# Kernel tuning notes

Measured on AMD Instinct MI355X. Metric: run time of the kernel, lower is better.

## Reference

```python
import jax, jax.numpy as jnp
import numpy as np

N = 50000       # nodes
E = 400000      # edges (before self-loops)
IN_C = 128
HID = 32        # hidden_channels per head
HEADS = 8
OUT_C = 64
K = 16          # num_clusters
NEG_SLOPE = 0.2
EPS = 1e-16


def setup_inputs() -> dict:
    key = jax.random.key(0)
    ks = jax.random.split(key, 14)
    g = lambda k, sh, sc: (jax.random.normal(k, sh, jnp.float32) * sc)
    return {
        "x": jax.random.normal(ks[0], (N, IN_C), jnp.float32),
        "edge_index": jax.random.randint(ks[1], (2, E), 0, N, dtype=jnp.int32),
        # GAT layer 1: in -> HEADS*HID
        "W1": g(ks[2], (IN_C, HEADS * HID), 0.08),
        "att_src1": g(ks[3], (HEADS, HID), 0.1),
        "att_dst1": g(ks[4], (HEADS, HID), 0.1),
        "b1": jnp.zeros((HEADS * HID,), jnp.float32),
        # GAT layer 2: HEADS*HID -> OUT_C, heads=1, concat=False
        "W2": g(ks[5], (HEADS * HID, OUT_C), 0.06),
        "att_src2": g(ks[6], (1, OUT_C), 0.1),
        "att_dst2": g(ks[7], (1, OUT_C), 0.1),
        "b2": jnp.zeros((OUT_C,), jnp.float32),
        # MLP head: OUT_C -> 128 -> K
        "Wm1": g(ks[8], (OUT_C, 128), 0.1),
        "bm1": jnp.zeros((128,), jnp.float32),
        "Wm2": g(ks[9], (128, K), 0.1),
        "bm2": jnp.zeros((K,), jnp.float32),
    }


def _gat_layer(x, W, att_src, att_dst, bias, src, dst, heads, ch, concat):
    # x: [N, F_in] -> h: [N, H, C]
    h = (x @ W).reshape(N, heads, ch)
    a_src = jnp.einsum('nhc,hc->nh', h, att_src)   # [N, H]
    a_dst = jnp.einsum('nhc,hc->nh', h, att_dst)   # [N, H]
    e = jax.nn.leaky_relu(a_src[src] + a_dst[dst], NEG_SLOPE)  # [Etot, H]
    # segment softmax over destination node
    m = jax.ops.segment_max(e, dst, num_segments=N)            # [N, H]
    ex = jnp.exp(e - m[dst])
    den = jax.ops.segment_sum(ex, dst, num_segments=N)         # [N, H]
    alpha = ex / (den[dst] + EPS)                              # [Etot, H]
    out = jax.ops.segment_sum(alpha[:, :, None] * h[src], dst, num_segments=N)  # [N, H, C]
    out = out.reshape(N, heads * ch) if concat else out.mean(axis=1)
    return out + bias


def reference(x, edge_index, W1, att_src1, att_dst1, b1, W2, att_src2, att_dst2, b2, Wm1, bm1, Wm2, bm2):
    # PyG GATConv adds self-loops by default
    loop = jnp.arange(N, dtype=edge_index.dtype)
    src = jnp.concatenate([edge_index[0], loop])
    dst = jnp.concatenate([edge_index[1], loop])
    # dropout layers are identity in eval mode
    h = jax.nn.elu(_gat_layer(x, W1, att_src1, att_dst1, b1, src, dst, HEADS, HID, True))
    embeddings = _gat_layer(h, W2, att_src2, att_dst2, b2, src, dst, 1, OUT_C, False)
    logits = jax.nn.relu(embeddings @ Wm1 + bm1) @ Wm2 + bm2
    s = jax.nn.softmax(logits, axis=1)
    return (s, embeddings)
```

## Files before the change

kernel.cpp:

```cpp
#include <hip/hip_runtime.h>
#include <hip/hip_fp16.h>
#include <math.h>

#define NNODES 50000
#define NEDGES 400000
#define INC    128
#define HC1    256
#define NHEADS 8
#define OUTC   64
#define NK     16
#define NEG_SLOPE 0.2f
#define EPS_F  1e-16f

typedef unsigned short u16;
typedef __attribute__((ext_vector_type(8))) short bf16x8;
typedef __attribute__((ext_vector_type(4))) float f32x4;

__device__ __forceinline__ float lrelu(float x){ return x > 0.f ? x : NEG_SLOPE * x; }
__device__ __forceinline__ float eluf(float x){ return x > 0.f ? x : (__expf(x) - 1.f); }
__device__ __forceinline__ float bf2f(u16 v){ return __uint_as_float((unsigned)v << 16); }
__device__ __forceinline__ u16 f2bf(float f){
    unsigned u = __float_as_uint(f);
    unsigned r = (u + 0x7FFFu + ((u >> 16) & 1u)) >> 16;
    return (u16)r;
}
__device__ __forceinline__ short f2bf_s(float f){ return (short)f2bf(f); }
__device__ __forceinline__ u16 f2h(float f){ return __half_as_ushort(__float2half(f)); }
__device__ __forceinline__ float h2f(u16 v){ return __half2float(__ushort_as_half(v)); }

__device__ __forceinline__ void fmix_lo(float& acc, unsigned w, float a){
    asm("v_fma_mix_f32 %0, %1, %2, %0 op_sel:[0,0,0] op_sel_hi:[1,0,0]"
        : "+v"(acc) : "v"(w), "v"(a));
}
__device__ __forceinline__ void fmix_hi(float& acc, unsigned w, float a){
    asm("v_fma_mix_f32 %0, %1, %2, %0 op_sel:[1,0,0] op_sel_hi:[1,0,0]"
        : "+v"(acc) : "v"(w), "v"(a));
}
__device__ __forceinline__ void mac8(float* acc, uint4 w, float a){
    fmix_lo(acc[0], w.x, a); fmix_hi(acc[1], w.x, a);
    fmix_lo(acc[2], w.y, a); fmix_hi(acc[3], w.y, a);
    fmix_lo(acc[4], w.z, a); fmix_hi(acc[5], w.z, a);
    fmix_lo(acc[6], w.w, a); fmix_hi(acc[7], w.w, a);
}
__device__ __forceinline__ void mac4(float4& acc, uint2 w, float a){
    fmix_lo(acc.x, w.x, a); fmix_hi(acc.y, w.x, a);
    fmix_lo(acc.z, w.y, a); fmix_hi(acc.w, w.y, a);
}

#define EB 1563
#define TB 232
__global__ void count_deg_tw_k(const int* __restrict__ dst, int* __restrict__ deg,
                               const float* __restrict__ W1, u16* __restrict__ W1t,
                               const float* __restrict__ W2, u16* __restrict__ W2t,
                               const float* __restrict__ Wm1, u16* __restrict__ W1mt,
                               const float* __restrict__ Wm2, u16* __restrict__ W2mt){
    if (blockIdx.x < EB){
        int e = blockIdx.x * 256 + threadIdx.x;
        if (e < NEDGES) atomicAdd(&deg[dst[e]], 1);
    } else {
        int i = (blockIdx.x - EB) * 256 + threadIdx.x;
        if (i < 32768){
            int n = i >> 7, k = i & 127;
            W1t[i] = f2bf(W1[k * 256 + n]);
        } else if (i < 49152){
            int ii = i - 32768;
            int n = ii >> 8, k = ii & 255;
            W2t[ii] = f2bf(W2[k * 64 + n]);
        } else if (i < 57344){
            int ii = i - 49152;
            int hd = ii >> 6, e = ii & 63;
            W1mt[ii] = f2bf(Wm1[e * 128 + hd]);
        } else if (i < 59392){
            int ii = i - 57344;
            int k = ii >> 7, hd = ii & 127;
            W2mt[ii] = f2bf(Wm2[hd * NK + k]);
        }
    }
}

__global__ void blocksum_k(const int* __restrict__ deg, int* __restrict__ bsum){
    __shared__ int sm[4];
    int i = blockIdx.x * 256 + threadIdx.x;
    int v = (i < NNODES) ? deg[i] : 0;
    for (int off = 1; off < 64; off <<= 1) v += __shfl_xor(v, off);
    int lane = threadIdx.x & 63, wid = threadIdx.x >> 6;
    if (lane == 0) sm[wid] = v;
    __syncthreads();
    if (threadIdx.x == 0) bsum[blockIdx.x] = sm[0] + sm[1] + sm[2] + sm[3];
}

__global__ void scan_write_k(const int* __restrict__ deg, const int* __restrict__ bsum,
                             int* __restrict__ rowptr){
    __shared__ int sm[4];
    __shared__ int sadd;
    int tid = threadIdx.x;
    int pv = (tid < blockIdx.x) ? bsum[tid] : 0;
    for (int off = 1; off < 64; off <<= 1) pv += __shfl_xor(pv, off);
    int lane = tid & 63, wid = tid >> 6;
    if (lane == 0) sm[wid] = pv;
    __syncthreads();
    if (tid == 0) sadd = sm[0] + sm[1] + sm[2] + sm[3];
    __syncthreads();

    int i = blockIdx.x * 256 + tid;
    int v = (i < NNODES) ? deg[i] : 0;
    int sv = v;
    for (int off = 1; off < 64; off <<= 1){ int t = __shfl_up(sv, off); if (lane >= off) sv += t; }
    __shared__ int wsum[4];
    if (lane == 63) wsum[wid] = sv;
    __syncthreads();
    int add = sadd;
    for (int w = 0; w < wid; w++) add += wsum[w];
    sv += add;
    if (i < NNODES) rowptr[i + 1] = sv;
    if (i == 0) rowptr[0] = 0;
}

__global__ void fill_csr_k(const int* __restrict__ src, const int* __restrict__ dst,
                           const int* __restrict__ rowptr, int* __restrict__ fillc,
                           int* __restrict__ col){
    int e = blockIdx.x * 256 + threadIdx.x;
    if (e < NEDGES){
        int d = dst[e];
        int pos = atomicAdd(&fillc[d], 1);
        col[rowptr[d] + pos] = src[e];
    }
}

__global__ __launch_bounds__(256, 4) void l1_k(const float* __restrict__ x, const u16* __restrict__ W1t,
                     const float* __restrict__ att_s, const float* __restrict__ att_d,
                     u16* __restrict__ h1b, float* __restrict__ as1, float* __restrict__ ad1){
    __shared__ u16 Bs[16384];
    int tid = threadIdx.x;
    int lane = tid & 63, wid = tid >> 6;
    int ln = lane & 15, quad = lane >> 4;
    int m0 = blockIdx.x * 64 + wid * 16;
    int nb = blockIdx.y * 128;
    int hb = blockIdx.y * 4;
    int arow = m0 + ln; if (arow >= NNODES) arow = NNODES - 1;

#pragma unroll
    for (int it = 0; it < 8; it++){
        int p = it * 256 + tid;
        int c = p >> 6, l = p & 63;
        int snt = c & 7, skt = c >> 3;
        int sln = l & 15, sq = l >> 4;
        uint4 v = *(const uint4*)(W1t + (size_t)(nb + snt * 16 + sln) * INC + skt * 32 + sq * 8);
        *(uint4*)(&Bs[p * 8]) = v;
    }

    bf16x8 a[4];
#pragma unroll
    for (int kt = 0; kt < 4; kt++){
        const float* ap = x + (size_t)arow * INC + kt * 32 + quad * 8;
        float4 v0 = *(const float4*)ap;
        float4 v1 = *(const float4*)(ap + 4);
        bf16x8 t;
        t[0] = f2bf_s(v0.x); t[1] = f2bf_s(v0.y); t[2] = f2bf_s(v0.z); t[3] = f2bf_s(v0.w);
        t[4] = f2bf_s(v1.x); t[5] = f2bf_s(v1.y); t[6] = f2bf_s(v1.z); t[7] = f2bf_s(v1.w);
        a[kt] = t;
    }

    __syncthreads();

    f32x4 acc[8];
#pragma unroll
    for (int nt = 0; nt < 8; nt++) acc[nt] = (f32x4){0.f, 0.f, 0.f, 0.f};

#pragma unroll
    for (int kt = 0; kt < 4; kt++){
#pragma unroll
        for (int nt = 0; nt < 8; nt++){
            bf16x8 b = *(const bf16x8*)(&Bs[(kt * 8 + nt) * 512 + lane * 8]);
            acc[nt] = __builtin_amdgcn_mfma_f32_16x16x32_bf16(a[kt], b, acc[nt], 0, 0, 0);
        }
    }

#pragma unroll
    for (int i = 0; i < 4; i++){
        int r = m0 + quad * 4 + i;
        if (r < NNODES){
#pragma unroll
            for (int nt = 0; nt < 8; nt++)
                h1b[(size_t)r * HC1 + nb + nt * 16 + ln] = f2h(acc[nt][i]);
        }
    }

#pragma unroll
    for (int i = 0; i < 4; i++){
        int r = m0 + quad * 4 + i;
        float ps_keep = 0.f, pd_keep = 0.f;
#pragma unroll
        for (int h = 0; h < 4; h++){
            float ps = acc[2 * h][i]     * att_s[nb + h * 32 + ln]
                     + acc[2 * h + 1][i] * att_s[nb + h * 32 + 16 + ln];
            float pd = acc[2 * h][i]     * att_d[nb + h * 32 + ln]
                     + acc[2 * h + 1][i] * att_d[nb + h * 32 + 16 + ln];
            ps += __shfl_xor(ps, 1); pd += __shfl_xor(pd, 1);
            ps += __shfl_xor(ps, 2); pd += __shfl_xor(pd, 2);
            ps += __shfl_xor(ps, 4); pd += __shfl_xor(pd, 4);
            ps += __shfl_xor(ps, 8); pd += __shfl_xor(pd, 8);
            if (ln == h){ ps_keep = ps; pd_keep = pd; }
        }
        if (ln < 4 && r < NNODES){
            as1[r * NHEADS + hb + ln] = ps_keep;
            ad1[r * NHEADS + hb + ln] = pd_keep;
        }
    }
}

__global__ __launch_bounds__(256, 4) void l2_k(const u16* __restrict__ hL1b, const u16* __restrict__ W2t,
                     const float* __restrict__ att_s, const float* __restrict__ att_d,
                     u16* __restrict__ h2b, float* __restrict__ as2, float* __restrict__ ad2){
    __shared__ u16 Bs[16384];
    int tid = threadIdx.x;
    int lane = tid & 63, wid = tid >> 6;
    int ln = lane & 15, quad = lane >> 4;
    int m0 = blockIdx.x * 64 + wid * 16;
    int arow = m0 + ln; if (arow >= NNODES) arow = NNODES - 1;

#pragma unroll
    for (int it = 0; it < 8; it++){
        int p = it * 256 + tid;
        int c = p >> 6, l = p & 63;
        int snt = c & 3, skt = c >> 2;
        int sln = l & 15, sq = l >> 4;
        uint4 v = *(const uint4*)(W2t + (size_t)(snt * 16 + sln) * HC1 + skt * 32 + sq * 8);
        *(uint4*)(&Bs[p * 8]) = v;
    }

    __syncthreads();

    f32x4 acc[4];
#pragma unroll
    for (int nt = 0; nt < 4; nt++) acc[nt] = (f32x4){0.f, 0.f, 0.f, 0.f};

#pragma unroll
    for (int kt = 0; kt < 8; kt++){
        bf16x8 a = *(const bf16x8*)(hL1b + (size_t)arow * HC1 + kt * 32 + quad * 8);
#pragma unroll
        for (int nt = 0; nt < 4; nt++){
            bf16x8 b = *(const bf16x8*)(&Bs[(kt * 4 + nt) * 512 + lane * 8]);
            acc[nt] = __builtin_amdgcn_mfma_f32_16x16x32_bf16(a, b, acc[nt], 0, 0, 0);
        }
    }

#pragma unroll
    for (int i = 0; i < 4; i++){
        int r = m0 + quad * 4 + i;
        if (r < NNODES){
#pragma unroll
            for (int nt = 0; nt < 4; nt++)
                h2b[(size_t)r * OUTC + nt * 16 + ln] = f2h(acc[nt][i]);
        }
        float ps = acc[0][i] * att_s[ln]      + acc[1][i] * att_s[16 + ln]
                 + acc[2][i] * att_s[32 + ln] + acc[3][i] * att_s[48 + ln];
        float pd = acc[0][i] * att_d[ln]      + acc[1][i] * att_d[16 + ln]
                 + acc[2][i] * att_d[32 + ln] + acc[3][i] * att_d[48 + ln];
        ps += __shfl_xor(ps, 1); pd += __shfl_xor(pd, 1);
        ps += __shfl_xor(ps, 2); pd += __shfl_xor(pd, 2);
        ps += __shfl_xor(ps, 4); pd += __shfl_xor(pd, 4);
        ps += __shfl_xor(ps, 8); pd += __shfl_xor(pd, 8);
        if (ln == 0 && r < NNODES){ as2[r] = ps; ad2[r] = pd; }
    }
}

__global__ void gat1_agg_k(const u16* __restrict__ h1b, const float* __restrict__ as1,
                           const float* __restrict__ ad1, const int* __restrict__ rowptr,
                           const int* __restrict__ col, const float* __restrict__ b1,
                           u16* __restrict__ outb){
    int lane = threadIdx.x & 63, wid = threadIdx.x >> 6;
    int d = blockIdx.x * 4 + wid;
    int row0 = rowptr[d];
    int deg  = rowptr[d + 1] - row0;

    int h8 = lane & 7, j = lane >> 3;
    float adst      = ad1[(unsigned)d * NHEADS + h8];
    float asrc_self = as1[(unsigned)d * NHEADS + h8];
    float e_self = lrelu(asrc_self + adst);

    if (deg <= 64){
        int nch = (deg + 7) >> 3;
        int cv[8]; float ex[8];
        float vmax = e_self;
#pragma unroll
        for (int c = 0; c < 8; c++){
            if (c >= nch) break;
            int idx = c * 8 + j;
            cv[c] = (idx < deg) ? col[row0 + idx] : d;
            if (idx < deg){
                float e = lrelu(as1[(unsigned)cv[c] * NHEADS + h8] + adst);
                ex[c] = e;
                vmax = fmaxf(vmax, e);
            } else ex[c] = -3e38f;
        }
        vmax = fmaxf(vmax, __shfl_xor(vmax, 8));
        vmax = fmaxf(vmax, __shfl_xor(vmax, 16));
        vmax = fmaxf(vmax, __shfl_xor(vmax, 32));

        float vsum = (j == 0) ? __expf(e_self - vmax) : 0.f;
#pragma unroll
        for (int c = 0; c < 8; c++){
            if (c >= nch) break;
            float t = (ex[c] > -1e37f) ? __expf(ex[c] - vmax) : 0.f;
            ex[c] = t;
            vsum += t;
        }
        vsum += __shfl_xor(vsum, 8);
        vsum += __shfl_xor(vsum, 16);
        vsum += __shfl_xor(vsum, 32);
        float rden = 1.f / (vsum + EPS_F);

        int hw = lane >> 5, l32 = lane & 31, hd = l32 >> 2;
        float sa_reg = __expf(e_self - vmax) * rden;
        float sa_b   = __shfl(sa_reg, hd);
        float asf    = hw ? 0.f : sa_b;

        float acc[8] = {0.f, 0.f, 0.f, 0.f, 0.f, 0.f, 0.f, 0.f};
        {
            uint4 w = *(const uint4*)(h1b + (unsigned)d * HC1 + (unsigned)(l32 * 8));
            mac8(acc, w, asf);
        }

#pragma unroll
        for (int c = 0; c < 8; c++){
            if (c >= nch) break;
            float an = ex[c] * rden;
            int s_arr[4]; float a_arr[4];
#pragma unroll
            for (int st = 0; st < 4; st++){
                int it = st * 2 + hw;
                s_arr[st] = __shfl(cv[c], it * 8);
                a_arr[st] = __shfl(an, it * 8 + hd);
            }
            uint4 w_arr[4];
#pragma unroll
            for (int st = 0; st < 4; st++)
                w_arr[st] = *(const uint4*)(h1b + (unsigned)s_arr[st] * HC1 + (unsigned)(l32 * 8));
#pragma unroll
            for (int st = 0; st < 4; st++) mac8(acc, w_arr[st], a_arr[st]);
        }
#pragma unroll
        for (int k = 0; k < 8; k++) acc[k] += __shfl_xor(acc[k], 32);

        if (lane < 32){
            float4 b0 = *(const float4*)(b1 + l32 * 8);
            float4 b4 = *(const float4*)(b1 + l32 * 8 + 4);
            uint4 o;
            o.x = (unsigned)f2bf(eluf(acc[0] + b0.x)) | ((unsigned)f2bf(eluf(acc[1] + b0.y)) << 16);
            o.y = (unsigned)f2bf(eluf(acc[2] + b0.z)) | ((unsigned)f2bf(eluf(acc[3] + b0.w)) << 16);
            o.z = (unsigned)f2bf(eluf(acc[4] + b4.x)) | ((unsigned)f2bf(eluf(acc[5] + b4.y)) << 16);
            o.w = (unsigned)f2bf(eluf(acc[6] + b4.z)) | ((unsigned)f2bf(eluf(acc[7] + b4.w)) << 16);
            *(uint4*)(outb + (size_t)d * HC1 + l32 * 8) = o;
        }
    } else {
        float vmax = e_self;
        for (int base = 0; base < deg; base += 8){
            int idx = base + j;
            if (idx < deg){
                int s = col[row0 + idx];
                vmax = fmaxf(vmax, lrelu(as1[(unsigned)s * NHEADS + h8] + adst));
            }
        }
        vmax = fmaxf(vmax, __shfl_xor(vmax, 8));
        vmax = fmaxf(vmax, __shfl_xor(vmax, 16));
        vmax = fmaxf(vmax, __shfl_xor(vmax, 32));

        float vsum = (j == 0) ? __expf(e_self - vmax) : 0.f;
        for (int base = 0; base < deg; base += 8){
            int idx = base + j;
            if (idx < deg){
                int s = col[row0 + idx];
                vsum += __expf(lrelu(as1[(unsigned)s * NHEADS + h8] + adst) - vmax);
            }
        }
        vsum += __shfl_xor(vsum, 8);
        vsum += __shfl_xor(vsum, 16);
        vsum += __shfl_xor(vsum, 32);
        float rden = 1.f / (vsum + EPS_F);

        int hw = lane >> 5, l32 = lane & 31, hd = l32 >> 2;
        float sa_reg = __expf(e_self - vmax) * rden;
        float sa_b   = __shfl(sa_reg, hd);
        float asf    = hw ? 0.f : sa_b;

        float acc[8] = {0.f, 0.f, 0.f, 0.f, 0.f, 0.f, 0.f, 0.f};
        {
            uint4 w = *(const uint4*)(h1b + (unsigned)d * HC1 + (unsigned)(l32 * 8));
            mac8(acc, w, asf);
        }

        for (int base = 0; base < deg; base += 8){
            int eidx = base + j;
            int cj = (eidx < deg) ? col[row0 + eidx] : d;
            float ae = (eidx < deg)
                     ? __expf(lrelu(as1[(unsigned)cj * NHEADS + h8] + adst) - vmax) * rden : 0.f;
            int s_arr[4]; float a_arr[4];
#pragma unroll
            for (int st = 0; st < 4; st++){
                int it = st * 2 + hw;
                s_arr[st] = __shfl(cj, it * 8);
                a_arr[st] = __shfl(ae, it * 8 + hd);
            }
            uint4 w_arr[4];
#pragma unroll
            for (int st = 0; st < 4; st++)
                w_arr[st] = *(const uint4*)(h1b + (unsigned)s_arr[st] * HC1 + (unsigned)(l32 * 8));
#pragma unroll
            for (int st = 0; st < 4; st++) mac8(acc, w_arr[st], a_arr[st]);
        }
#pragma unroll
        for (int k = 0; k < 8; k++) acc[k] += __shfl_xor(acc[k], 32);

        if (lane < 32){
            float4 b0 = *(const float4*)(b1 + l32 * 8);
            float4 b4 = *(const float4*)(b1 + l32 * 8 + 4);
            uint4 o;
            o.x = (unsigned)f2bf(eluf(acc[0] + b0.x)) | ((unsigned)f2bf(eluf(acc[1] + b0.y)) << 16);
            o.y = (unsigned)f2bf(eluf(acc[2] + b0.z)) | ((unsigned)f2bf(eluf(acc[3] + b0.w)) << 16);
            o.z = (unsigned)f2bf(eluf(acc[4] + b4.x)) | ((unsigned)f2bf(eluf(acc[5] + b4.y)) << 16);
            o.w = (unsigned)f2bf(eluf(acc[6] + b4.z)) | ((unsigned)f2bf(eluf(acc[7] + b4.w)) << 16);
            *(uint4*)(outb + (size_t)d * HC1 + l32 * 8) = o;
        }
    }
}

__global__ void gat2_agg_k(const u16* __restrict__ h2b, const float* __restrict__ as2,
                           const float* __restrict__ ad2, const int* __restrict__ rowptr,
                           const int* __restrict__ col, const float* __restrict__ b2,
                           float* __restrict__ emb){
    int lane = threadIdx.x & 63, wid = threadIdx.x >> 6;
    int d = blockIdx.x * 4 + wid;
    int row0 = rowptr[d];
    int deg  = rowptr[d + 1] - row0;

    float adst = ad2[d];
    float e_self = lrelu(as2[d] + adst);

    if (deg <= 64){
        int sv = (lane < deg) ? col[row0 + lane] : d;
        float e_lane = (lane < deg) ? lrelu(as2[sv] + adst) : -3e38f;
        float vmax = fmaxf(e_self, e_lane);
        for (int m = 1; m < 64; m <<= 1) vmax = fmaxf(vmax, __shfl_xor(vmax, m));
        float exl = (lane < deg) ? __expf(e_lane - vmax) : 0.f;
        float vsum = exl + ((lane == 0) ? __expf(e_self - vmax) : 0.f);
        for (int m = 1; m < 64; m <<= 1) vsum += __shfl_xor(vsum, m);
        float rden = 1.f / (vsum + EPS_F);
        float alpha_l = exl * rden;
        float sa = __expf(e_self - vmax) * rden;

        int q = lane >> 4, c4 = (lane & 15) * 4;
        float a0 = (q == 0) ? sa : 0.f;
        float4 acc = make_float4(0.f, 0.f, 0.f, 0.f);
        {
            uint2 w = *(const uint2*)(h2b + (unsigned)d * OUTC + c4);
            mac4(acc, w, a0);
        }
        for (int it0 = 0; it0 < deg; it0 += 16){
            int s_arr[4]; float a_arr[4];
#pragma unroll
            for (int k = 0; k < 4; k++){
                int itc = min(it0 + k * 4 + q, 63);
                s_arr[k] = __shfl(sv, itc);
                a_arr[k] = __shfl(alpha_l, itc);
            }
            uint2 w_arr[4];
#pragma unroll
            for (int k = 0; k < 4; k++)
                w_arr[k] = *(const uint2*)(h2b + (unsigned)s_arr[k] * OUTC + c4);
#pragma unroll
            for (int k = 0; k < 4; k++) mac4(acc, w_arr[k], a_arr[k]);
        }
        acc.x += __shfl_xor(acc.x, 16); acc.y += __shfl_xor(acc.y, 16);
        acc.z += __shfl_xor(acc.z, 16); acc.w += __shfl_xor(acc.w, 16);
        acc.x += __shfl_xor(acc.x, 32); acc.y += __shfl_xor(acc.y, 32);
        acc.z += __shfl_xor(acc.z, 32); acc.w += __shfl_xor(acc.w, 32);
        if (lane < 16){
            float4 bb = *(const float4*)(b2 + c4);
            float4 o = make_float4(acc.x + bb.x, acc.y + bb.y, acc.z + bb.z, acc.w + bb.w);
            *(float4*)(emb + (size_t)d * OUTC + c4) = o;
        }
    } else {
        float vmax = e_self;
        for (int base = 0; base < deg; base += 64){
            int idx = base + lane;
            if (idx < deg){
                int s = col[row0 + idx];
                vmax = fmaxf(vmax, lrelu(as2[s] + adst));
            }
        }
        for (int m = 1; m < 64; m <<= 1) vmax = fmaxf(vmax, __shfl_xor(vmax, m));
        float vsum = (lane == 0) ? __expf(e_self - vmax) : 0.f;
        for (int base = 0; base < deg; base += 64){
            int idx = base + lane;
            if (idx < deg){
                int s = col[row0 + idx];
                vsum += __expf(lrelu(as2[s] + adst) - vmax);
            }
        }
        for (int m = 1; m < 64; m <<= 1) vsum += __shfl_xor(vsum, m);
        float rden = 1.f / (vsum + EPS_F);
        float alpha = __expf(e_self - vmax) * rden;
        float acc = alpha * h2f(h2b[(unsigned)d * OUTC + lane]);
        for (int idx = 0; idx < deg; idx++){
            int s = col[row0 + idx];
            float a = __expf(lrelu(as2[s] + adst) - vmax) * rden;
            acc += a * h2f(h2b[(unsigned)s * OUTC + lane]);
        }
        emb[(size_t)d * OUTC + lane] = acc + b2[lane];
    }
}

__global__ void mlp_mfma_k(const float* __restrict__ emb, const u16* __restrict__ W1mt,
                           const float* __restrict__ bm1, const u16* __restrict__ W2mt,
                           const float* __restrict__ bm2, float* __restrict__ sout){
    __shared__ u16 hid[4][16][136];
    int lane = threadIdx.x & 63, wid = threadIdx.x >> 6;
    int ln = lane & 15, quad = lane >> 4;
    int m0 = blockIdx.x * 64 + wid * 16;
    int arow = m0 + ln; if (arow >= NNODES) arow = NNODES - 1;

    bf16x8 a[2];
#pragma unroll
    for (int kt = 0; kt < 2; kt++){
        const float* ap = emb + (size_t)arow * OUTC + kt * 32 + quad * 8;
        float4 v0 = *(const float4*)ap;
        float4 v1 = *(const float4*)(ap + 4);
        bf16x8 t;
        t[0] = f2bf_s(v0.x); t[1] = f2bf_s(v0.y); t[2] = f2bf_s(v0.z); t[3] = f2bf_s(v0.w);
        t[4] = f2bf_s(v1.x); t[5] = f2bf_s(v1.y); t[6] = f2bf_s(v1.z); t[7] = f2bf_s(v1.w);
        a[kt] = t;
    }

    f32x4 acc[8];
#pragma unroll
    for (int nt = 0; nt < 8; nt++) acc[nt] = (f32x4){0.f, 0.f, 0.f, 0.f};
#pragma unroll
    for (int kt = 0; kt < 2; kt++){
#pragma unroll
        for (int nt = 0; nt < 8; nt++){
            bf16x8 b = *(const bf16x8*)(W1mt + (size_t)(nt * 16 + ln) * OUTC + kt * 32 + quad * 8);
            acc[nt] = __builtin_amdgcn_mfma_f32_16x16x32_bf16(a[kt], b, acc[nt], 0, 0, 0);
        }
    }

#pragma unroll
    for (int nt = 0; nt < 8; nt++){
        float bb = bm1[nt * 16 + ln];
#pragma unroll
        for (int i = 0; i < 4; i++){
            float h = fmaxf(acc[nt][i] + bb, 0.f);
            hid[wid][quad * 4 + i][nt * 16 + ln] = f2bf(h);
        }
    }

    f32x4 acc2 = (f32x4){0.f, 0.f, 0.f, 0.f};
#pragma unroll
    for (int kt = 0; kt < 4; kt++){
        bf16x8 ah = *(const bf16x8*)&hid[wid][ln][kt * 32 + quad * 8];
        bf16x8 bw = *(const bf16x8*)(W2mt + (size_t)ln * 128 + kt * 32 + quad * 8);
        acc2 = __builtin_amdgcn_mfma_f32_16x16x32_bf16(ah, bw, acc2, 0, 0, 0);
    }

    float bcl = bm2[ln];
#pragma unroll
    for (int i = 0; i < 4; i++){
        int r = m0 + quad * 4 + i;
        float lg = acc2[i] + bcl;
        float m = lg;
        m = fmaxf(m, __shfl_xor(m, 1));
        m = fmaxf(m, __shfl_xor(m, 2));
        m = fmaxf(m, __shfl_xor(m, 4));
        m = fmaxf(m, __shfl_xor(m, 8));
        float ex = expf(lg - m);
        float s = ex;
        s += __shfl_xor(s, 1);
        s += __shfl_xor(s, 2);
        s += __shfl_xor(s, 4);
        s += __shfl_xor(s, 8);
        if (r < NNODES) sout[(size_t)r * NK + ln] = ex / s;
    }
}

extern "C" void kernel_launch(void* const* d_in, const int* in_sizes, int n_in,
                              void* d_out, int out_size, void* d_ws, size_t ws_size,
                              hipStream_t stream){
    const float* x      = (const float*)d_in[0];
    const int*   ei     = (const int*)d_in[1];
    const int*   srcv   = ei;
    const int*   dstv   = ei + NEDGES;
    const float* W1     = (const float*)d_in[2];
    const float* att_s1 = (const float*)d_in[3];
    const float* att_d1 = (const float*)d_in[4];
    const float* b1     = (const float*)d_in[5];
    const float* W2     = (const float*)d_in[6];
    const float* att_s2 = (const float*)d_in[7];
    const float* att_d2 = (const float*)d_in[8];
    const float* b2     = (const float*)d_in[9];
    const float* Wm1    = (const float*)d_in[10];
    const float* bm1    = (const float*)d_in[11];
    const float* Wm2    = (const float*)d_in[12];
    const float* bm2    = (const float*)d_in[13];

    float* out     = (float*)d_out;
    float* emb_out = out + (size_t)NNODES * NK;

    u16* h1b   = (u16*)d_ws;
    u16* hL1b  = h1b  + (size_t)NNODES * HC1;
    u16* h2b   = hL1b + (size_t)NNODES * HC1;
    u16* W1t   = h2b  + (size_t)NNODES * OUTC;
    u16* W2t   = W1t + 256 * 128;
    u16* W1mt  = W2t + 64 * 256;
    u16* W2mt  = W1mt + 128 * 64;
    float* as1 = (float*)(W2mt + 16 * 128);
    float* ad1 = as1 + (size_t)NNODES * NHEADS;
    float* as2 = ad1 + (size_t)NNODES * NHEADS;
    float* ad2 = as2 + NNODES;
    int* deg    = (int*)(ad2 + NNODES);
    int* fillc  = deg + NNODES;
    int* rowptr = fillc + NNODES;
    int* bsum   = rowptr + NNODES + 1;
    int* colv   = bsum + 256;

    hipMemsetAsync(deg, 0, 2 * NNODES * sizeof(int), stream);

    const int NB = (NNODES + 255) / 256;

    count_deg_tw_k<<<EB + TB, 256, 0, stream>>>(dstv, deg, W1, W1t, W2, W2t, Wm1, W1mt, Wm2, W2mt);
    blocksum_k<<<NB, 256, 0, stream>>>(deg, bsum);
    scan_write_k<<<NB, 256, 0, stream>>>(deg, bsum, rowptr);
    fill_csr_k<<<(NEDGES + 255) / 256, 256, 0, stream>>>(srcv, dstv, rowptr, fillc, colv);

    const int MB = (NNODES + 63) / 64;

    l1_k<<<dim3(MB, 2), 256, 0, stream>>>(x, W1t, att_s1, att_d1, h1b, as1, ad1);
    gat1_agg_k<<<NNODES / 4, 256, 0, stream>>>(h1b, as1, ad1, rowptr, colv, b1, hL1b);

    l2_k<<<MB, 256, 0, stream>>>(hL1b, W2t, att_s2, att_d2, h2b, as2, ad2);
    gat2_agg_k<<<NNODES / 4, 256, 0, stream>>>(h2b, as2, ad2, rowptr, colv, b2, emb_out);

    mlp_mfma_k<<<MB, 256, 0, stream>>>(emb_out, W1mt, bm1, W2mt, bm2, out);
}
```

Measured before the change: 251.0 us.

## Use head-major layout for layer-1 features and split aggregation per head

Layer-1 projected features, attention scores and aggregated outputs are stored head-major ([head][node][32]) instead of node-major. The layer-1 aggregation kernel now gives each head its own block and handles one destination node with 8 lanes, gathering 64-byte per-head rows, so the working set touched per head is smaller and more cache friendly. Layer 2's A-operand loads are adjusted to the new layout. The layer-2 aggregation also issues the first 16 neighbour gathers before the softmax reductions so their latency overlaps. The trade-off is shorter per-edge gathers, extra launch blocks, and a serial per-lane loop for nodes with more than 16 neighbours.

```diff
diff --git a/kernel.cpp b/kernel.cpp
--- a/kernel.cpp
+++ b/kernel.cpp
@@ -129,7 +129,7 @@
 
 __global__ __launch_bounds__(256, 4) void l1_k(const float* __restrict__ x, const u16* __restrict__ W1t,
                      const float* __restrict__ att_s, const float* __restrict__ att_d,
-                     u16* __restrict__ h1b, float* __restrict__ as1, float* __restrict__ ad1){
+                     u16* __restrict__ h1bh, float* __restrict__ as1h, float* __restrict__ ad1h){
     __shared__ u16 Bs[16384];
     int tid = threadIdx.x;
     int lane = tid & 63, wid = tid >> 6;
@@ -181,8 +181,11 @@
         int r = m0 + quad * 4 + i;
         if (r < NNODES){
 #pragma unroll
-            for (int nt = 0; nt < 8; nt++)
-                h1b[(size_t)r * HC1 + nb + nt * 16 + ln] = f2h(acc[nt][i]);
+            for (int nt = 0; nt < 8; nt++){
+                int c  = nb + nt * 16 + ln;
+                int hh = c >> 5, c5 = c & 31;
+                h1bh[((size_t)hh * NNODES + r) * 32 + c5] = f2h(acc[nt][i]);
+            }
         }
     }
 
@@ -203,8 +206,8 @@
             if (ln == h){ ps_keep = ps; pd_keep = pd; }
         }
         if (ln < 4 && r < NNODES){
-            as1[r * NHEADS + hb + ln] = ps_keep;
-            ad1[r * NHEADS + hb + ln] = pd_keep;
+            as1h[(size_t)(hb + ln) * NNODES + r] = ps_keep;
+            ad1h[(size_t)(hb + ln) * NNODES + r] = pd_keep;
         }
     }
 }
@@ -237,7 +240,7 @@
 
 #pragma unroll
     for (int kt = 0; kt < 8; kt++){
-        bf16x8 a = *(const bf16x8*)(hL1b + (size_t)arow * HC1 + kt * 32 + quad * 8);
+        bf16x8 a = *(const bf16x8*)(hL1b + ((size_t)kt * NNODES + arow) * 32 + quad * 8);
 #pragma unroll
         for (int nt = 0; nt < 4; nt++){
             bf16x8 b = *(const bf16x8*)(&Bs[(kt * 4 + nt) * 512 + lane * 8]);
@@ -265,163 +268,110 @@
     }
 }
 
-__global__ void gat1_agg_k(const u16* __restrict__ h1b, const float* __restrict__ as1,
-                           const float* __restrict__ ad1, const int* __restrict__ rowptr,
+__global__ void gat1_agg_k(const u16* __restrict__ h1bh, const float* __restrict__ as1h,
+                           const float* __restrict__ ad1h, const int* __restrict__ rowptr,
                            const int* __restrict__ col, const float* __restrict__ b1,
                            u16* __restrict__ outb){
     int lane = threadIdx.x & 63, wid = threadIdx.x >> 6;
-    int d = blockIdx.x * 4 + wid;
-    int row0 = rowptr[d];
-    int deg  = rowptr[d + 1] - row0;
-
-    int h8 = lane & 7, j = lane >> 3;
-    float adst      = ad1[(unsigned)d * NHEADS + h8];
-    float asrc_self = as1[(unsigned)d * NHEADS + h8];
-    float e_self = lrelu(asrc_self + adst);
-
-    if (deg <= 64){
-        int nch = (deg + 7) >> 3;
-        int cv[8]; float ex[8];
-        float vmax = e_self;
-#pragma unroll
-        for (int c = 0; c < 8; c++){
-            if (c >= nch) break;
-            int idx = c * 8 + j;
-            cv[c] = (idx < deg) ? col[row0 + idx] : d;
-            if (idx < deg){
-                float e = lrelu(as1[(unsigned)cv[c] * NHEADS + h8] + adst);
-                ex[c] = e;
-                vmax = fmaxf(vmax, e);
-            } else ex[c] = -3e38f;
-        }
-        vmax = fmaxf(vmax, __shfl_xor(vmax, 8));
-        vmax = fmaxf(vmax, __shfl_xor(vmax, 16));
-        vmax = fmaxf(vmax, __shfl_xor(vmax, 32));
-
-        float vsum = (j == 0) ? __expf(e_self - vmax) : 0.f;
-#pragma unroll
-        for (int c = 0; c < 8; c++){
-            if (c >= nch) break;
-            float t = (ex[c] > -1e37f) ? __expf(ex[c] - vmax) : 0.f;
-            ex[c] = t;
-            vsum += t;
-        }
-        vsum += __shfl_xor(vsum, 8);
-        vsum += __shfl_xor(vsum, 16);
-        vsum += __shfl_xor(vsum, 32);
-        float rden = 1.f / (vsum + EPS_F);
-
-        int hw = lane >> 5, l32 = lane & 31, hd = l32 >> 2;
-        float sa_reg = __expf(e_self - vmax) * rden;
-        float sa_b   = __shfl(sa_reg, hd);
-        float asf    = hw ? 0.f : sa_b;
-
-        float acc[8] = {0.f, 0.f, 0.f, 0.f, 0.f, 0.f, 0.f, 0.f};
-        {
-            uint4 w = *(const uint4*)(h1b + (unsigned)d * HC1 + (unsigned)(l32 * 8));
-            mac8(acc, w, asf);
-        }
-
-#pragma unroll
-        for (int c = 0; c < 8; c++){
-            if (c >= nch) break;
-            float an = ex[c] * rden;
-            int s_arr[4]; float a_arr[4];
-#pragma unroll
-            for (int st = 0; st < 4; st++){
-                int it = st * 2 + hw;
-                s_arr[st] = __shfl(cv[c], it * 8);
-                a_arr[st] = __shfl(an, it * 8 + hd);
-            }
-            uint4 w_arr[4];
-#pragma unroll
-            for (int st = 0; st < 4; st++)
-                w_arr[st] = *(const uint4*)(h1b + (unsigned)s_arr[st] * HC1 + (unsigned)(l32 * 8));
-#pragma unroll
-            for (int st = 0; st < 4; st++) mac8(acc, w_arr[st], a_arr[st]);
-        }
-#pragma unroll
-        for (int k = 0; k < 8; k++) acc[k] += __shfl_xor(acc[k], 32);
-
-        if (lane < 32){
-            float4 b0 = *(const float4*)(b1 + l32 * 8);
-            float4 b4 = *(const float4*)(b1 + l32 * 8 + 4);
-            uint4 o;
-            o.x = (unsigned)f2bf(eluf(acc[0] + b0.x)) | ((unsigned)f2bf(eluf(acc[1] + b0.y)) << 16);
-            o.y = (unsigned)f2bf(eluf(acc[2] + b0.z)) | ((unsigned)f2bf(eluf(acc[3] + b0.w)) << 16);
-            o.z = (unsigned)f2bf(eluf(acc[4] + b4.x)) | ((unsigned)f2bf(eluf(acc[5] + b4.y)) << 16);
-            o.w = (unsigned)f2bf(eluf(acc[6] + b4.z)) | ((unsigned)f2bf(eluf(acc[7] + b4.w)) << 16);
-            *(uint4*)(outb + (size_t)d * HC1 + l32 * 8) = o;
-        }
-    } else {
-        float vmax = e_self;
-        for (int base = 0; base < deg; base += 8){
-            int idx = base + j;
-            if (idx < deg){
-                int s = col[row0 + idx];
-                vmax = fmaxf(vmax, lrelu(as1[(unsigned)s * NHEADS + h8] + adst));
-            }
-        }
-        vmax = fmaxf(vmax, __shfl_xor(vmax, 8));
-        vmax = fmaxf(vmax, __shfl_xor(vmax, 16));
-        vmax = fmaxf(vmax, __shfl_xor(vmax, 32));
-
-        float vsum = (j == 0) ? __expf(e_self - vmax) : 0.f;
-        for (int base = 0; base < deg; base += 8){
-            int idx = base + j;
-            if (idx < deg){
-                int s = col[row0 + idx];
-                vsum += __expf(lrelu(as1[(unsigned)s * NHEADS + h8] + adst) - vmax);
-            }
-        }
-        vsum += __shfl_xor(vsum, 8);
-        vsum += __shfl_xor(vsum, 16);
-        vsum += __shfl_xor(vsum, 32);
-        float rden = 1.f / (vsum + EPS_F);
-
-        int hw = lane >> 5, l32 = lane & 31, hd = l32 >> 2;
-        float sa_reg = __expf(e_self - vmax) * rden;
-        float sa_b   = __shfl(sa_reg, hd);
-        float asf    = hw ? 0.f : sa_b;
-
-        float acc[8] = {0.f, 0.f, 0.f, 0.f, 0.f, 0.f, 0.f, 0.f};
-        {
-            uint4 w = *(const uint4*)(h1b + (unsigned)d * HC1 + (unsigned)(l32 * 8));
-            mac8(acc, w, asf);
-        }
-
-        for (int base = 0; base < deg; base += 8){
-            int eidx = base + j;
-            int cj = (eidx < deg) ? col[row0 + eidx] : d;
-            float ae = (eidx < deg)
-                     ? __expf(lrelu(as1[(unsigned)cj * NHEADS + h8] + adst) - vmax) * rden : 0.f;
-            int s_arr[4]; float a_arr[4];
-#pragma unroll
-            for (int st = 0; st < 4; st++){
-                int it = st * 2 + hw;
-                s_arr[st] = __shfl(cj, it * 8);
-                a_arr[st] = __shfl(ae, it * 8 + hd);
-            }
-            uint4 w_arr[4];
-#pragma unroll
-            for (int st = 0; st < 4; st++)
-                w_arr[st] = *(const uint4*)(h1b + (unsigned)s_arr[st] * HC1 + (unsigned)(l32 * 8));
-#pragma unroll
-            for (int st = 0; st < 4; st++) mac8(acc, w_arr[st], a_arr[st]);
-        }
-#pragma unroll
-        for (int k = 0; k < 8; k++) acc[k] += __shfl_xor(acc[k], 32);
-
-        if (lane < 32){
-            float4 b0 = *(const float4*)(b1 + l32 * 8);
-            float4 b4 = *(const float4*)(b1 + l32 * 8 + 4);
-            uint4 o;
-            o.x = (unsigned)f2bf(eluf(acc[0] + b0.x)) | ((unsigned)f2bf(eluf(acc[1] + b0.y)) << 16);
-            o.y = (unsigned)f2bf(eluf(acc[2] + b0.z)) | ((unsigned)f2bf(eluf(acc[3] + b0.w)) << 16);
-            o.z = (unsigned)f2bf(eluf(acc[4] + b4.x)) | ((unsigned)f2bf(eluf(acc[5] + b4.y)) << 16);
-            o.w = (unsigned)f2bf(eluf(acc[6] + b4.z)) | ((unsigned)f2bf(eluf(acc[7] + b4.w)) << 16);
-            *(uint4*)(outb + (size_t)d * HC1 + l32 * 8) = o;
-        }
+    int g = lane >> 3, t = lane & 7;
+    int h = blockIdx.x & 7;
+    int d = (blockIdx.x >> 3) * 32 + wid * 8 + g;
+    bool valid = (d < NNODES);
+    int dd = valid ? d : (NNODES - 1);
+    int row0 = rowptr[dd];
+    int deg  = rowptr[dd + 1] - row0;
+
+    const float* ash = as1h + (size_t)h * NNODES;
+    float adst = ad1h[(size_t)h * NNODES + dd];
+    float e_self = lrelu(ash[dd] + adst);
+    const u16* hb = h1bh + (size_t)h * NNODES * 32;
+
+    int sv0 = (t < deg)     ? col[row0 + t]     : dd;
+    int sv1 = (8 + t < deg) ? col[row0 + 8 + t] : dd;
+    float ev0 = ash[sv0];
+    float ev1 = ash[sv1];
+    uint2 wself = *(const uint2*)(hb + (size_t)dd * 32 + t * 4);
+
+    float e0 = (t < deg)     ? lrelu(ev0 + adst) : -3e38f;
+    float e1 = (8 + t < deg) ? lrelu(ev1 + adst) : -3e38f;
+    float vmax = fmaxf(e_self, fmaxf(e0, e1));
+    if (deg > 16){
+        for (int idx = 16 + t; idx < deg; idx += 8){
+            int s = col[row0 + idx];
+            vmax = fmaxf(vmax, lrelu(ash[s] + adst));
+        }
+    }
+    vmax = fmaxf(vmax, __shfl_xor(vmax, 1));
+    vmax = fmaxf(vmax, __shfl_xor(vmax, 2));
+    vmax = fmaxf(vmax, __shfl_xor(vmax, 4));
+
+    float x0 = (t < deg)     ? __expf(e0 - vmax) : 0.f;
+    float x1 = (8 + t < deg) ? __expf(e1 - vmax) : 0.f;
+    float vsum = x0 + x1 + ((t == 0) ? __expf(e_self - vmax) : 0.f);
+    if (deg > 16){
+        for (int idx = 16 + t; idx < deg; idx += 8){
+            int s = col[row0 + idx];
+            vsum += __expf(lrelu(ash[s] + adst) - vmax);
+        }
+    }
+    vsum += __shfl_xor(vsum, 1);
+    vsum += __shfl_xor(vsum, 2);
+    vsum += __shfl_xor(vsum, 4);
+    float rden = 1.f / (vsum + EPS_F);
+
+    float4 acc = make_float4(0.f, 0.f, 0.f, 0.f);
+    mac4(acc, wself, __expf(e_self - vmax) * rden);
+
+    int gb = g * 8;
+    if (deg > 0){
+        int s_arr[4]; float a_arr[4]; uint2 w_arr[4];
+#pragma unroll
+        for (int j = 0; j < 4; j++){ s_arr[j] = __shfl(sv0, gb + j); a_arr[j] = __shfl(x0, gb + j) * rden; }
+#pragma unroll
+        for (int j = 0; j < 4; j++) w_arr[j] = *(const uint2*)(hb + (size_t)s_arr[j] * 32 + t * 4);
+#pragma unroll
+        for (int j = 0; j < 4; j++) mac4(acc, w_arr[j], a_arr[j]);
+        if (deg > 4){
+#pragma unroll
+            for (int j = 0; j < 4; j++){ s_arr[j] = __shfl(sv0, gb + 4 + j); a_arr[j] = __shfl(x0, gb + 4 + j) * rden; }
+#pragma unroll
+            for (int j = 0; j < 4; j++) w_arr[j] = *(const uint2*)(hb + (size_t)s_arr[j] * 32 + t * 4);
+#pragma unroll
+            for (int j = 0; j < 4; j++) mac4(acc, w_arr[j], a_arr[j]);
+        }
+    }
+    if (deg > 8){
+        int s_arr[4]; float a_arr[4]; uint2 w_arr[4];
+#pragma unroll
+        for (int j = 0; j < 4; j++){ s_arr[j] = __shfl(sv1, gb + j); a_arr[j] = __shfl(x1, gb + j) * rden; }
+#pragma unroll
+        for (int j = 0; j < 4; j++) w_arr[j] = *(const uint2*)(hb + (size_t)s_arr[j] * 32 + t * 4);
+#pragma unroll
+        for (int j = 0; j < 4; j++) mac4(acc, w_arr[j], a_arr[j]);
+        if (deg > 12){
+#pragma unroll
+            for (int j = 0; j < 4; j++){ s_arr[j] = __shfl(sv1, gb + 4 + j); a_arr[j] = __shfl(x1, gb + 4 + j) * rden; }
+#pragma unroll
+            for (int j = 0; j < 4; j++) w_arr[j] = *(const uint2*)(hb + (size_t)s_arr[j] * 32 + t * 4);
+#pragma unroll
+            for (int j = 0; j < 4; j++) mac4(acc, w_arr[j], a_arr[j]);
+        }
+    }
+    if (deg > 16){
+        for (int idx = 16; idx < deg; idx++){
+            int s = col[row0 + idx];
+            float a = __expf(lrelu(ash[s] + adst) - vmax) * rden;
+            uint2 w = *(const uint2*)(hb + (size_t)s * 32 + t * 4);
+            mac4(acc, w, a);
+        }
+    }
+
+    if (valid){
+        float4 bb = *(const float4*)(b1 + h * 32 + t * 4);
+        uint2 o;
+        o.x = (unsigned)f2bf(eluf(acc.x + bb.x)) | ((unsigned)f2bf(eluf(acc.y + bb.y)) << 16);
+        o.y = (unsigned)f2bf(eluf(acc.z + bb.z)) | ((unsigned)f2bf(eluf(acc.w + bb.w)) << 16);
+        *(uint2*)(outb + ((size_t)h * NNODES + d) * 32 + t * 4) = o;
     }
 }
 
@@ -439,7 +389,18 @@
 
     if (deg <= 64){
         int sv = (lane < deg) ? col[row0 + lane] : d;
-        float e_lane = (lane < deg) ? lrelu(as2[sv] + adst) : -3e38f;
+        float e_raw = as2[sv];
+
+        int q = lane >> 4, c4 = (lane & 15) * 4;
+        uint2 wself = *(const uint2*)(h2b + (unsigned)d * OUTC + c4);
+        uint2 wpre[4];
+#pragma unroll
+        for (int k = 0; k < 4; k++){
+            int s = __shfl(sv, k * 4 + q);
+            wpre[k] = *(const uint2*)(h2b + (unsigned)s * OUTC + c4);
+        }
+
+        float e_lane = (lane < deg) ? lrelu(e_raw + adst) : -3e38f;
         float vmax = fmaxf(e_self, e_lane);
         for (int m = 1; m < 64; m <<= 1) vmax = fmaxf(vmax, __shfl_xor(vmax, m));
         float exl = (lane < deg) ? __expf(e_lane - vmax) : 0.f;
@@ -449,14 +410,17 @@
         float alpha_l = exl * rden;
         float sa = __expf(e_self - vmax) * rden;
 
-        int q = lane >> 4, c4 = (lane & 15) * 4;
         float a0 = (q == 0) ? sa : 0.f;
         float4 acc = make_float4(0.f, 0.f, 0.f, 0.f);
+        mac4(acc, wself, a0);
         {
-            uint2 w = *(const uint2*)(h2b + (unsigned)d * OUTC + c4);
-            mac4(acc, w, a0);
-        }
-        for (int it0 = 0; it0 < deg; it0 += 16){
+            float a_arr[4];
+#pragma unroll
+            for (int k = 0; k < 4; k++) a_arr[k] = __shfl(alpha_l, k * 4 + q);
+#pragma unroll
+            for (int k = 0; k < 4; k++) mac4(acc, wpre[k], a_arr[k]);
+        }
+        for (int it0 = 16; it0 < deg; it0 += 16){
             int s_arr[4]; float a_arr[4];
 #pragma unroll
             for (int k = 0; k < 4; k++){
@@ -634,7 +598,7 @@
     const int MB = (NNODES + 63) / 64;
 
     l1_k<<<dim3(MB, 2), 256, 0, stream>>>(x, W1t, att_s1, att_d1, h1b, as1, ad1);
-    gat1_agg_k<<<NNODES / 4, 256, 0, stream>>>(h1b, as1, ad1, rowptr, colv, b1, hL1b);
+    gat1_agg_k<<<8 * ((NNODES + 31) / 32), 256, 0, stream>>>(h1b, as1, ad1, rowptr, colv, b1, hL1b);
 
     l2_k<<<MB, 256, 0, stream>>>(hL1b, W2t, att_s2, att_d2, h2b, as2, ad2);
     gat2_agg_k<<<NNODES / 4, 256, 0, stream>>>(h2b, as2, ad2, rowptr, colv, b2, emb_out);
```

Result: no change. 249.6 us (-0.6%).
